# Optimization experiments

Hardware: AMD Instinct MI355X
Metric: run time of the kernel (lower is better)

The kernel has to match this reference:

```python
import jax, jax.numpy as jnp
import numpy as np

HEADS = 12
HEAD_DIM = 64          # dim_out // heads = 768 // 12
Q_STRIDE = 4
WINDOW_SIZE = 16       # post-pool tokens per window; pre-pool = Q_STRIDE*WINDOW_SIZE = 64
DIM = 768
DIM_OUT = 768


def setup_inputs() -> dict:
    key = jax.random.key(0)
    k1, k2, k3 = jax.random.split(key, 3)
    B, N = 32, 3136
    x = jax.random.normal(k1, (B, N, DIM), dtype=jnp.float32)
    Wqkv = jax.random.normal(k2, (DIM, 3 * DIM_OUT), dtype=jnp.float32) * 0.02
    bqkv = jnp.zeros((3 * DIM_OUT,), dtype=jnp.float32)
    Wproj = jax.random.normal(k3, (DIM_OUT, DIM_OUT), dtype=jnp.float32) * 0.02
    bproj = jnp.zeros((DIM_OUT,), dtype=jnp.float32)
    return {"x": x, "Wqkv": Wqkv, "bqkv": bqkv, "Wproj": Wproj, "bproj": bproj}


def reference(x, Wqkv, bqkv, Wproj, bproj):
    B, N, _ = x.shape
    num_windows = N // (Q_STRIDE * WINDOW_SIZE)  # 49
    scale = HEAD_DIM ** (-0.5)

    # QKV projection (torch Linear uses x @ W^T; here Wqkv is stored [dim, 3*dim_out])
    qkv = x @ Wqkv + bqkv                                  # [B, N, 3*dim_out]
    # Same reshape as torch: windows are the inner split of the token axis
    qkv = qkv.reshape(B, N // num_windows, num_windows, 3, HEADS, HEAD_DIM)
    qkv = jnp.transpose(qkv, (3, 0, 4, 2, 1, 5))           # [3, B, h, w, t, d]
    q, k, v = qkv[0], qkv[1], qkv[2]                       # t = Q_STRIDE*WINDOW_SIZE

    # Query max-pooling over stride groups
    q = q.reshape(B, HEADS, num_windows, Q_STRIDE, WINDOW_SIZE, HEAD_DIM).max(axis=3)
    # q: [B, h, w, WINDOW_SIZE, d]

    # Scaled dot-product attention within each window
    logits = jnp.einsum('bhwqd,bhwkd->bhwqk', q, k) * scale
    attn = jax.nn.softmax(logits, axis=-1)
    o = jnp.einsum('bhwqk,bhwkd->bhwqd', attn, v)          # [B, h, w, q, d]

    # transpose(1,3) then flatten tokens, channels = heads*head_dim
    o = jnp.transpose(o, (0, 3, 2, 1, 4)).reshape(B, -1, DIM_OUT)
    return o @ Wproj + bproj
```

## Files before the change

kernel.cpp:

```cpp
#include <hip/hip_runtime.h>
#include <hip/hip_bf16.h>


typedef __bf16 bf16x8 __attribute__((ext_vector_type(8)));
typedef float f32x4 __attribute__((ext_vector_type(4)));
typedef unsigned short u16x8 __attribute__((ext_vector_type(8)));

#define GLOBAL_AS __attribute__((address_space(1)))
#define LDS_AS __attribute__((address_space(3)))

__device__ __forceinline__ unsigned short f2bf(float f) {
    unsigned u = __builtin_bit_cast(unsigned, f);
    u += 0x7FFFu + ((u >> 16) & 1u);
    return (unsigned short)(u >> 16);
}
__device__ __forceinline__ float bf2f(unsigned short h) {
    return __builtin_bit_cast(float, (unsigned)h << 16);
}

__device__ __forceinline__ void load16_to_lds(const void* g, void* l) {
    __builtin_amdgcn_global_load_lds((const GLOBAL_AS unsigned int*)g,
                                     (LDS_AS unsigned int*)l, 16, 0, 0);
}

__global__ void cvt_f32_bf16(const float* __restrict__ in,
                             unsigned short* __restrict__ out, long n4) {
    long i = (long)blockIdx.x * blockDim.x + threadIdx.x;
    if (i >= n4) return;
    float4 f = ((const float4*)in)[i];
    uint2 u;
    u.x = (unsigned)f2bf(f.x) | ((unsigned)f2bf(f.y) << 16);
    u.y = (unsigned)f2bf(f.z) | ((unsigned)f2bf(f.w) << 16);
    ((uint2*)out)[i] = u;
}

__global__ void transpose_cvt(const float* __restrict__ W,
                              unsigned short* __restrict__ Wt, int K, int N) {
    __shared__ float tile[32][33];
    int bx = blockIdx.x * 32;
    int by = blockIdx.y * 32;
    int tx = threadIdx.x & 31, ty = threadIdx.x >> 5;
    #pragma unroll
    for (int i = 0; i < 32; i += 8)
        tile[ty + i][tx] = W[(size_t)(by + ty + i) * N + bx + tx];
    __syncthreads();
    #pragma unroll
    for (int i = 0; i < 32; i += 8)
        Wt[(size_t)(bx + ty + i) * K + by + tx] = f2bf(tile[tx][ty + i]);
}

#define VM_WAIT2 asm volatile("s_waitcnt vmcnt(2)" ::: "memory")
#define VM_WAIT0 asm volatile("s_waitcnt vmcnt(0)" ::: "memory")

#define GPHASE(BUF, CSW, IH, LOADBG, STG, WAITS) do {                        \
    if (LOADBG) {                                                            \
        const unsigned short* bb = &ls[(BUF) * 32768 + 16384 + (CSW)];       \
        bg[0] = *(const bf16x8*)&bb[(wn +  0 + lane15) * 64];                \
        bg[1] = *(const bf16x8*)&bb[(wn + 16 + lane15) * 64];                \
        bg[2] = *(const bf16x8*)&bb[(wn + 32 + lane15) * 64];                \
        bg[3] = *(const bf16x8*)&bb[(wn + 48 + lane15) * 64];                \
    }                                                                        \
    {                                                                        \
        const unsigned short* ab = &ls[(BUF) * 32768 + (CSW)];               \
        af[0] = *(const bf16x8*)&ab[(wm + (IH)*64 +  0 + lane15) * 64];      \
        af[1] = *(const bf16x8*)&ab[(wm + (IH)*64 + 16 + lane15) * 64];      \
        af[2] = *(const bf16x8*)&ab[(wm + (IH)*64 + 32 + lane15) * 64];      \
        af[3] = *(const bf16x8*)&ab[(wm + (IH)*64 + 48 + lane15) * 64];      \
    }                                                                        \
    STG;                                                                     \
    WAITS;                                                                   \
    __builtin_amdgcn_s_barrier();                                            \
    asm volatile("s_waitcnt lgkmcnt(0)" ::: "memory");                       \
    __builtin_amdgcn_sched_barrier(0);                                       \
    __builtin_amdgcn_s_setprio(1);                                           \
    _Pragma("unroll")                                                        \
    for (int ii = 0; ii < 4; ++ii)                                           \
        _Pragma("unroll")                                                    \
        for (int j = 0; j < 4; ++j)                                          \
            acc[(IH)*4 + ii][j] = __builtin_amdgcn_mfma_f32_16x16x32_bf16(   \
                bg[j], af[ii], acc[(IH)*4 + ii][j], 0, 0, 0);                \
    __builtin_amdgcn_s_setprio(0);                                           \
    __builtin_amdgcn_s_barrier();                                            \
} while (0)

template <bool OUT_BF16>
__global__ __launch_bounds__(512, 2)
void gemm_bt256(const unsigned short* __restrict__ A,
                const unsigned short* __restrict__ Bt,
                const float* __restrict__ bias,
                void* __restrict__ Cv, int M, int N, int K) {
    __shared__ alignas(16) unsigned short ls[65536];

    const int tid  = threadIdx.x;
    const int lane = tid & 63;
    const int wave = tid >> 6;
    const int wm = (wave >> 2) * 128;
    const int wn = (wave & 3) * 64;
    const int lane15 = lane & 15;
    const int quad   = lane >> 4;
    const int csw0 = ((quad    ) ^ (lane & 7)) * 8;
    const int csw1 = ((quad + 4) ^ (lane & 7)) * 8;

    const int nwg = (int)(gridDim.x * gridDim.y);
    const int hid = (int)(blockIdx.y * gridDim.x + blockIdx.x);
    const int q8  = nwg >> 3, r8 = nwg & 7;
    const int xcd = hid & 7;
    const int lid = (xcd < r8 ? xcd * (q8 + 1) : r8 * (q8 + 1) + (xcd - r8) * q8)
                    + (hid >> 3);
    const int tileX = lid % (int)gridDim.x;
    const int tileY = lid / (int)gridDim.x;
    const long bm = (long)tileY * 256;
    const long bn = (long)tileX * 256;

    const int r0 = tid >> 3;
    const int lc = (tid & 7) ^ (r0 & 7);
    const unsigned short* gA = A  + (bm + r0) * (long)K + lc * 8;
    const unsigned short* gB = Bt + (bn + r0) * (long)K + lc * 8;
    const int ldsWaveBase = wave * 512;

    auto STAGE_A = [&](int buf, int q, int kt) {
        load16_to_lds(gA + (long)q * 64 * K + kt * 64,
                      &ls[buf * 32768 + q * 4096 + ldsWaveBase]);
    };
    auto STAGE_B = [&](int buf, int q, int kt) {
        load16_to_lds(gB + (long)q * 64 * K + kt * 64,
                      &ls[buf * 32768 + 16384 + q * 4096 + ldsWaveBase]);
    };

    f32x4 acc[8][4] = {};
    bf16x8 af[4], bg[4];

    const int NT = K >> 6;
    const int NI = NT >> 1;

    STAGE_A(0, 0, 0); STAGE_A(0, 1, 0); STAGE_A(0, 2, 0); STAGE_A(0, 3, 0);
    STAGE_B(0, 0, 0); STAGE_B(0, 1, 0); STAGE_B(0, 2, 0); STAGE_B(0, 3, 0);
    STAGE_A(1, 0, 1); STAGE_A(1, 2, 1);
    VM_WAIT2;
    __builtin_amdgcn_s_barrier();

    for (int i = 0; i < NI; ++i) {
        const int t2 = 2 * i;
        const bool last = (i == NI - 1);
        GPHASE(0, csw0, 0, 1,
               { STAGE_A(1, 1, t2 + 1); STAGE_A(1, 3, t2 + 1); STAGE_B(1, 0, t2 + 1); },
               { (void)0; });
        GPHASE(0, csw0, 1, 0,
               { STAGE_B(1, 1, t2 + 1); STAGE_B(1, 2, t2 + 1); STAGE_B(1, 3, t2 + 1); },
               { (void)0; });
        GPHASE(0, csw1, 0, 1, { (void)0; }, { (void)0; });
        GPHASE(0, csw1, 1, 0,
               { if (!last) { STAGE_A(0, 0, t2 + 2); STAGE_A(0, 2, t2 + 2); } },
               { if (last) { VM_WAIT0; } else { VM_WAIT2; } });
        GPHASE(1, csw0, 0, 1,
               { if (!last) { STAGE_A(0, 1, t2 + 2); STAGE_A(0, 3, t2 + 2); } },
               { (void)0; });
        GPHASE(1, csw0, 1, 0,
               { if (!last) { STAGE_B(0, 0, t2 + 2); STAGE_B(0, 1, t2 + 2); } },
               { (void)0; });
        GPHASE(1, csw1, 0, 1,
               { if (!last) { STAGE_B(0, 2, t2 + 2); STAGE_B(0, 3, t2 + 2); } },
               { (void)0; });
        GPHASE(1, csw1, 1, 0,
               { if (!last) { STAGE_A(1, 0, t2 + 3); STAGE_A(1, 2, t2 + 3); VM_WAIT2; } },
               { (void)0; });
    }

    const long rbase = bm + wm + lane15;
    const int  cbase = (int)bn + wn + quad * 4;
    #pragma unroll
    for (int j = 0; j < 4; ++j) {
        const int col = cbase + j * 16;
        const float4 bv = *(const float4*)&bias[col];
        #pragma unroll
        for (int i = 0; i < 8; ++i) {
            const long row = rbase + i * 16;
            const size_t idx = (size_t)row * N + col;
            const float v0 = acc[i][j][0] + bv.x;
            const float v1 = acc[i][j][1] + bv.y;
            const float v2 = acc[i][j][2] + bv.z;
            const float v3 = acc[i][j][3] + bv.w;
            if constexpr (OUT_BF16) {
                ushort4 s;
                s.x = f2bf(v0); s.y = f2bf(v1); s.z = f2bf(v2); s.w = f2bf(v3);
                *(ushort4*)((unsigned short*)Cv + idx) = s;
            } else {
                float4 s;
                s.x = v0; s.y = v1; s.z = v2; s.w = v3;
                *(float4*)((float*)Cv + idx) = s;
            }
        }
    }
}

__global__ __launch_bounds__(256)
void attn_win_mfma(const unsigned short* __restrict__ qkv,
                   unsigned short* __restrict__ o) {
    const int hg = blockIdx.x;
    const int w  = blockIdx.y;
    const int b  = blockIdx.z;
    const int wave = threadIdx.x >> 6;
    const int lane = threadIdx.x & 63;
    const int h = hg * 4 + wave;
    const int l = lane & 15;
    const int quad = lane >> 4;

    __shared__ alignas(16) unsigned short vT[4][64 * 72];
    __shared__ alignas(16) unsigned short ps[4][16 * 72];

    const long tokStride = 49L * 2304;
    const long base = ((long)b * 3136 + w) * 2304 + h * 64;

    bf16x8 af[2];
    {
        const unsigned short* qr = qkv + base + (long)l * tokStride + quad * 8;
        float m0[8], m1[8];
        #pragma unroll
        for (int sg = 0; sg < 4; ++sg) {
            uint4 u0 = *(const uint4*)(qr + (long)sg * 16 * tokStride);
            uint4 u1 = *(const uint4*)(qr + (long)sg * 16 * tokStride + 32);
            const unsigned short* p0 = (const unsigned short*)&u0;
            const unsigned short* p1 = (const unsigned short*)&u1;
            #pragma unroll
            for (int e = 0; e < 8; ++e) {
                float f0 = bf2f(p0[e]), f1 = bf2f(p1[e]);
                if (sg == 0) { m0[e] = f0; m1[e] = f1; }
                else { m0[e] = fmaxf(m0[e], f0); m1[e] = fmaxf(m1[e], f1); }
            }
        }
        u16x8 a0, a1;
        #pragma unroll
        for (int e = 0; e < 8; ++e) {
            a0[e] = f2bf(m0[e] * 0.125f);
            a1[e] = f2bf(m1[e] * 0.125f);
        }
        af[0] = __builtin_bit_cast(bf16x8, a0);
        af[1] = __builtin_bit_cast(bf16x8, a1);
    }

    {
        const unsigned short* vr = qkv + base + (long)lane * tokStride + 1536;
        unsigned short* vw = &vT[wave][0];
        #pragma unroll
        for (int i = 0; i < 8; ++i) {
            uint4 u = *(const uint4*)(vr + i * 8);
            const unsigned short* pe = (const unsigned short*)&u;
            #pragma unroll
            for (int e = 0; e < 8; ++e)
                vw[(i * 8 + e) * 72 + lane] = pe[e];
        }
    }

    f32x4 Sc[4] = {};
    {
        bf16x8 bk0, bk1;
        #pragma unroll
        for (int tt = 0; tt < 4; ++tt) {
            const unsigned short* kr =
                qkv + base + (long)(tt * 16 + l) * tokStride + 768 + quad * 8;
            bk0 = __builtin_bit_cast(bf16x8, *(const uint4*)kr);
            bk1 = __builtin_bit_cast(bf16x8, *(const uint4*)(kr + 32));
            Sc[tt] = __builtin_amdgcn_mfma_f32_16x16x32_bf16(af[0], bk0, Sc[tt], 0, 0, 0);
            Sc[tt] = __builtin_amdgcn_mfma_f32_16x16x32_bf16(af[1], bk1, Sc[tt], 0, 0, 0);
        }
    }

    float pr[4][4];
    {
        #pragma unroll
        for (int r = 0; r < 4; ++r) {
            float mx = fmaxf(fmaxf(Sc[0][r], Sc[1][r]), fmaxf(Sc[2][r], Sc[3][r]));
            #pragma unroll
            for (int off = 1; off < 16; off <<= 1)
                mx = fmaxf(mx, __shfl_xor(mx, off));
            float sum = 0.f;
            #pragma unroll
            for (int tt = 0; tt < 4; ++tt) {
                pr[tt][r] = __expf(Sc[tt][r] - mx);
                sum += pr[tt][r];
            }
            #pragma unroll
            for (int off = 1; off < 16; off <<= 1)
                sum += __shfl_xor(sum, off);
            const float inv = 1.0f / sum;
            #pragma unroll
            for (int tt = 0; tt < 4; ++tt) pr[tt][r] *= inv;
        }
    }

    {
        unsigned short* pw = &ps[wave][0];
        #pragma unroll
        for (int r = 0; r < 4; ++r)
            #pragma unroll
            for (int tt = 0; tt < 4; ++tt)
                pw[(quad * 4 + r) * 72 + tt * 16 + l] = f2bf(pr[tt][r]);
    }

    f32x4 Oc[4] = {};
    {
        #pragma unroll
        for (int s = 0; s < 2; ++s) {
            bf16x8 ap = *(const bf16x8*)&ps[wave][l * 72 + s * 32 + quad * 8];
            #pragma unroll
            for (int tt = 0; tt < 4; ++tt) {
                bf16x8 bv = *(const bf16x8*)&vT[wave][(tt * 16 + l) * 72 + s * 32 + quad * 8];
                Oc[tt] = __builtin_amdgcn_mfma_f32_16x16x32_bf16(ap, bv, Oc[tt], 0, 0, 0);
            }
        }
    }

    {
        const long obase = ((long)b * 784 + (long)(quad * 4) * 49 + w) * 768 + h * 64 + l;
        #pragma unroll
        for (int tt = 0; tt < 4; ++tt)
            #pragma unroll
            for (int r = 0; r < 4; ++r)
                o[obase + (long)r * 49 * 768 + tt * 16] = f2bf(Oc[tt][r]);
    }
}

extern "C" void kernel_launch(void* const* d_in, const int* in_sizes, int n_in,
                              void* d_out, int out_size, void* d_ws, size_t ws_size,
                              hipStream_t stream) {
    const float* x     = (const float*)d_in[0];
    const float* Wqkv  = (const float*)d_in[1];
    const float* bqkv  = (const float*)d_in[2];
    const float* Wproj = (const float*)d_in[3];
    const float* bproj = (const float*)d_in[4];
    float* out = (float*)d_out;

    const long needed1 = (32L * 3136 * 768 + 32L * 3136 * 2304 +
                          25088L * 768 + 2304L * 768 + 768L * 768) * 2;
    const int C  = (ws_size >= (size_t)needed1) ? 1 : 4;
    const int CB = 32 / C;
    const long XC = (long)CB * 3136 * 768;
    const long QC = (long)CB * 3136 * 2304;

    char* p = (char*)d_ws;
    unsigned short* xb    = (unsigned short*)p; p += XC * 2;
    unsigned short* qkvb  = (unsigned short*)p; p += QC * 2;
    unsigned short* ob    = (unsigned short*)p; p += 25088L * 768 * 2;
    unsigned short* WqkvT = (unsigned short*)p; p += 2304L * 768 * 2;
    unsigned short* WprojT= (unsigned short*)p; p += 768L * 768 * 2;

    transpose_cvt<<<dim3(72, 24), 256, 0, stream>>>(Wqkv, WqkvT, 768, 2304);
    transpose_cvt<<<dim3(24, 24), 256, 0, stream>>>(Wproj, WprojT, 768, 768);

    const int M = CB * 3136;
    for (int c = 0; c < C; ++c) {
        cvt_f32_bf16<<<(int)(XC / 4 / 256), 256, 0, stream>>>(x + (size_t)c * XC, xb, XC / 4);
        gemm_bt256<true><<<dim3(9, M / 256), 512, 0, stream>>>(
            xb, WqkvT, bqkv, qkvb, M, 2304, 768);
        attn_win_mfma<<<dim3(3, 49, CB), 256, 0, stream>>>(
            qkvb, ob + (size_t)c * CB * 784 * 768);
    }
    gemm_bt256<false><<<dim3(3, 98), 512, 0, stream>>>(
        ob, WprojT, bproj, out, 25088, 768, 768);
}
```

Measured before the change: 1.091 ms.

## Permute tokens into window-major order and write QKV in per-head window slabs

Input conversion now reorders tokens so each window's 64 tokens are contiguous. The QKV GEMM epilogue scatters its output into a [batch, window, section, head, token, dim] slab layout. The attention kernel then reads q/k/v as contiguous 64x64 blocks instead of strided tokens 49*2304 elements apart, which is meant to cut uncoalesced global reads. The QKV GEMM is split into two launches over half-M with an mBase offset. The cost is more index arithmetic in the converter and epilogue, plus scattered row writes in the GEMM store.

```diff
diff --git a/kernel.cpp b/kernel.cpp
--- a/kernel.cpp
+++ b/kernel.cpp
@@ -23,15 +23,21 @@
                                      (LDS_AS unsigned int*)l, 16, 0, 0);
 }
 
-__global__ void cvt_f32_bf16(const float* __restrict__ in,
-                             unsigned short* __restrict__ out, long n4) {
-    long i = (long)blockIdx.x * blockDim.x + threadIdx.x;
-    if (i >= n4) return;
-    float4 f = ((const float4*)in)[i];
+__global__ void cvt_permute(const float* __restrict__ in,
+                            unsigned short* __restrict__ out, int nRows) {
+    const long idx = (long)blockIdx.x * blockDim.x + threadIdx.x;
+    if (idx >= (long)nRows * 192) return;
+    const int g  = (int)(idx / 192);
+    const int c4 = (int)(idx - (long)g * 192);
+    const int b  = g / 3136;
+    const int nn = g - b * 3136;
+    const int t  = nn / 49;
+    const int w  = nn - t * 49;
+    float4 f = ((const float4*)in)[idx];
     uint2 u;
     u.x = (unsigned)f2bf(f.x) | ((unsigned)f2bf(f.y) << 16);
     u.y = (unsigned)f2bf(f.z) | ((unsigned)f2bf(f.w) << 16);
-    ((uint2*)out)[i] = u;
+    ((uint2*)out)[(long)(b * 3136 + w * 64 + t) * 192 + c4] = u;
 }
 
 __global__ void transpose_cvt(const float* __restrict__ W,
@@ -88,7 +94,7 @@
 void gemm_bt256(const unsigned short* __restrict__ A,
                 const unsigned short* __restrict__ Bt,
                 const float* __restrict__ bias,
-                void* __restrict__ Cv, int M, int N, int K) {
+                void* __restrict__ Cv, int mBase, int N, int K) {
     __shared__ alignas(16) unsigned short ls[65536];
 
     const int tid  = threadIdx.x;
@@ -166,27 +172,49 @@
                { (void)0; });
     }
 
-    const long rbase = bm + wm + lane15;
-    const int  cbase = (int)bn + wn + quad * 4;
-    #pragma unroll
-    for (int j = 0; j < 4; ++j) {
-        const int col = cbase + j * 16;
-        const float4 bv = *(const float4*)&bias[col];
+    const int rbase = (int)(bm) + wm + lane15;
+    if constexpr (OUT_BF16) {
+        const int colBase = (int)bn + wn;
+        const int sec = colBase / 768;
+        const int hh  = (colBase - sec * 768) >> 6;
+        const long shOff = (long)sec * 49152 + hh * 4096 + quad * 4;
+        unsigned short* qout = (unsigned short*)Cv;
+        float4 bv[4];
+        #pragma unroll
+        for (int j = 0; j < 4; ++j)
+            bv[j] = *(const float4*)&bias[colBase + quad * 4 + j * 16];
         #pragma unroll
         for (int i = 0; i < 8; ++i) {
-            const long row = rbase + i * 16;
-            const size_t idx = (size_t)row * N + col;
-            const float v0 = acc[i][j][0] + bv.x;
-            const float v1 = acc[i][j][1] + bv.y;
-            const float v2 = acc[i][j][2] + bv.z;
-            const float v3 = acc[i][j][3] + bv.w;
-            if constexpr (OUT_BF16) {
+            const int m  = mBase + rbase + i * 16;
+            const int b  = m / 3136;
+            const int r3 = m - b * 3136;
+            unsigned short* rp = qout + (long)(b * 49 + (r3 >> 6)) * 147456
+                                      + shOff + (long)(r3 & 63) * 64;
+            #pragma unroll
+            for (int j = 0; j < 4; ++j) {
                 ushort4 s;
-                s.x = f2bf(v0); s.y = f2bf(v1); s.z = f2bf(v2); s.w = f2bf(v3);
-                *(ushort4*)((unsigned short*)Cv + idx) = s;
-            } else {
+                s.x = f2bf(acc[i][j][0] + bv[j].x);
+                s.y = f2bf(acc[i][j][1] + bv[j].y);
+                s.z = f2bf(acc[i][j][2] + bv[j].z);
+                s.w = f2bf(acc[i][j][3] + bv[j].w);
+                *(ushort4*)(rp + j * 16) = s;
+            }
+        }
+    } else {
+        const int cbase = (int)bn + wn + quad * 4;
+        #pragma unroll
+        for (int j = 0; j < 4; ++j) {
+            const int col = cbase + j * 16;
+            const float4 bv = *(const float4*)&bias[col];
+            #pragma unroll
+            for (int i = 0; i < 8; ++i) {
+                const long row = (long)mBase + rbase + i * 16;
+                const size_t idx = (size_t)row * N + col;
                 float4 s;
-                s.x = v0; s.y = v1; s.z = v2; s.w = v3;
+                s.x = acc[i][j][0] + bv.x;
+                s.y = acc[i][j][1] + bv.y;
+                s.z = acc[i][j][2] + bv.z;
+                s.w = acc[i][j][3] + bv.w;
                 *(float4*)((float*)Cv + idx) = s;
             }
         }
@@ -208,17 +236,17 @@
     __shared__ alignas(16) unsigned short vT[4][64 * 72];
     __shared__ alignas(16) unsigned short ps[4][16 * 72];
 
-    const long tokStride = 49L * 2304;
-    const long base = ((long)b * 3136 + w) * 2304 + h * 64;
+    const long slab = (long)(b * 49 + w) * 147456;
+    const long hOff = (long)h * 4096;
 
     bf16x8 af[2];
     {
-        const unsigned short* qr = qkv + base + (long)l * tokStride + quad * 8;
+        const unsigned short* qr = qkv + slab + hOff + (long)l * 64 + quad * 8;
         float m0[8], m1[8];
         #pragma unroll
         for (int sg = 0; sg < 4; ++sg) {
-            uint4 u0 = *(const uint4*)(qr + (long)sg * 16 * tokStride);
-            uint4 u1 = *(const uint4*)(qr + (long)sg * 16 * tokStride + 32);
+            uint4 u0 = *(const uint4*)(qr + sg * 1024);
+            uint4 u1 = *(const uint4*)(qr + sg * 1024 + 32);
             const unsigned short* p0 = (const unsigned short*)&u0;
             const unsigned short* p1 = (const unsigned short*)&u1;
             #pragma unroll
@@ -239,7 +267,7 @@
     }
 
     {
-        const unsigned short* vr = qkv + base + (long)lane * tokStride + 1536;
+        const unsigned short* vr = qkv + slab + 98304 + hOff + (long)lane * 64;
         unsigned short* vw = &vT[wave][0];
         #pragma unroll
         for (int i = 0; i < 8; ++i) {
@@ -257,7 +285,7 @@
         #pragma unroll
         for (int tt = 0; tt < 4; ++tt) {
             const unsigned short* kr =
-                qkv + base + (long)(tt * 16 + l) * tokStride + 768 + quad * 8;
+                qkv + slab + 49152 + hOff + (long)(tt * 16 + l) * 64 + quad * 8;
             bk0 = __builtin_bit_cast(bf16x8, *(const uint4*)kr);
             bk1 = __builtin_bit_cast(bf16x8, *(const uint4*)(kr + 32));
             Sc[tt] = __builtin_amdgcn_mfma_f32_16x16x32_bf16(af[0], bk0, Sc[tt], 0, 0, 0);
@@ -347,14 +375,19 @@
     transpose_cvt<<<dim3(72, 24), 256, 0, stream>>>(Wqkv, WqkvT, 768, 2304);
     transpose_cvt<<<dim3(24, 24), 256, 0, stream>>>(Wproj, WprojT, 768, 768);
 
-    const int M = CB * 3136;
+    const int M  = CB * 3136;
+    const int Mh = M / 2;
     for (int c = 0; c < C; ++c) {
-        cvt_f32_bf16<<<(int)(XC / 4 / 256), 256, 0, stream>>>(x + (size_t)c * XC, xb, XC / 4);
-        gemm_bt256<true><<<dim3(9, M / 256), 512, 0, stream>>>(
-            xb, WqkvT, bqkv, qkvb, M, 2304, 768);
+        const int nRows = M;
+        cvt_permute<<<(int)(((long)nRows * 192 + 255) / 256), 256, 0, stream>>>(
+            x + (size_t)c * XC, xb, nRows);
+        gemm_bt256<true><<<dim3(9, Mh / 256), 512, 0, stream>>>(
+            xb, WqkvT, bqkv, qkvb, 0, 2304, 768);
+        gemm_bt256<true><<<dim3(9, Mh / 256), 512, 0, stream>>>(
+            xb + (long)Mh * 768, WqkvT, bqkv, qkvb, Mh, 2304, 768);
         attn_win_mfma<<<dim3(3, 49, CB), 256, 0, stream>>>(
             qkvb, ob + (size_t)c * CB * 784 * 768);
     }
     gemm_bt256<false><<<dim3(3, 98), 512, 0, stream>>>(
-        ob, WprojT, bproj, out, 25088, 768, 768);
-}
+        ob, WprojT, bproj, out, 0, 768, 768);
+}
```

Measured after the change: 1.068 ms. -2.1%, faster.
